# Performance work log

Measured on AMD Instinct MI355X. Metric: run time of the kernel, lower is better.

The kernel has to match this reference:

```python
import jax, jax.numpy as jnp
import numpy as np


def _hippo_dplr(n):
    # HiPPO-LegS -> NPLR -> DPLR (diagonal plus low rank) init, as in S4
    pr = np.sqrt(1.0 + 2.0 * np.arange(n))
    A = -(np.tril(pr[:, None] * pr[None, :]) - np.diag(np.arange(n)))
    p = np.sqrt(np.arange(n) + 0.5)
    b = np.sqrt(2.0 * np.arange(n) + 1.0)
    S = A + p[:, None] * p[None, :]
    lam_re = np.full(n, np.mean(np.diagonal(S)))
    lam_im, V = np.linalg.eigh(S * -1j)  # S*-1j is Hermitian
    p_c = V.conj().T @ p.astype(np.complex128)
    b_c = V.conj().T @ b.astype(np.complex128)
    return lam_re, lam_im, p_c, b_c


def setup_inputs():
    B, L, H, N = 4, 1024, 512, 64
    key = jax.random.key(0)
    kx, kc, ks, k1, k2 = jax.random.split(key, 5)
    lam_re, lam_im, p_c, b_c = _hippo_dplr(N)
    c = jax.random.normal(kc, (N, 2)) * (0.5 ** 0.5)
    f32 = lambda a: jnp.asarray(a, dtype=jnp.float32)
    return {
        'x': jax.random.normal(kx, (B, L, H), dtype=jnp.float32),
        'norm_weight': jnp.ones((H,), jnp.float32),
        'norm_bias': jnp.zeros((H,), jnp.float32),
        'lambda_re': f32(lam_re), 'lambda_im': f32(lam_im),
        'p_re': f32(p_c.real), 'p_im': f32(p_c.imag),
        'b_re': f32(b_c.real), 'b_im': f32(b_c.imag),
        'c_re': c[:, 0].astype(jnp.float32), 'c_im': c[:, 1].astype(jnp.float32),
        'd': jnp.ones((), jnp.float32),
        'log_step': jax.random.uniform(ks, (), jnp.float32, float(np.log(0.001)), float(np.log(0.1))),
        'out_w': (jax.random.normal(k1, (H, H), jnp.float32) / np.sqrt(H)).astype(jnp.float32),
        'out_b': jnp.zeros((H,), jnp.float32),
        'out2_w': (jax.random.normal(k2, (H, H), jnp.float32) / np.sqrt(H)).astype(jnp.float32),
        'out2_b': jnp.zeros((H,), jnp.float32),
    }


def reference(x, norm_weight, norm_bias, lambda_re, lambda_im, p_re, p_im,
              b_re, b_im, c_re, c_im, d, log_step, out_w, out_b, out2_w, out2_b):
    Bsz, L, H = x.shape
    skip = x
    # LayerNorm over channel dim (eps=1e-5, eqx default)
    mu = jnp.mean(x, -1, keepdims=True)
    var = jnp.mean((x - mu) ** 2, -1, keepdims=True)
    xn = (x - mu) / jnp.sqrt(var + 1e-5) * norm_weight + norm_bias
    # --- S4 DPLR bilinear discretization ---
    lam = (lambda_re + 1j * lambda_im).astype(jnp.complex64)
    p = (p_re + 1j * p_im).astype(jnp.complex64)
    b = (b_re + 1j * b_im).astype(jnp.complex64)
    c = (c_re + 1j * c_im).astype(jnp.complex64)
    step = jnp.exp(log_step).astype(jnp.complex64)
    N = lam.shape[0]
    I = jnp.eye(N, dtype=jnp.complex64)
    A = jnp.diag(lam) - p[:, None] * p[None, :].conj()
    A0 = (2.0 / step) * I + A
    Dinv = jnp.diag(1.0 / ((2.0 / step) - lam))
    qcD = p.conj()[None, :] @ Dinv           # [1,N]
    Dp = Dinv @ p[:, None]                   # [N,1]
    A1 = Dinv - (Dp @ qcD) / (1.0 + (qcD @ p[:, None]))  # Woodbury
    Ab = A1 @ A0                             # [N,N] discrete state matrix
    Bb = 2.0 * (A1 @ b[:, None])[:, 0]       # [N]
    # --- sequential state-space scan over time, vectorized over (B,H) lanes ---
    u = xn.astype(jnp.complex64)             # [B,L,H]

    def step_fn(state, u_t):                 # state: [B,H,N], u_t: [B,H]
        new = jnp.einsum('nm,bhm->bhn', Ab, state) + u_t[..., None] * Bb
        return new, jnp.einsum('n,bhn->bh', c, new).real

    init = jnp.zeros((Bsz, H, N), jnp.complex64)
    _, ys = jax.lax.scan(step_fn, init, jnp.moveaxis(u, 1, 0))  # ys: [L,B,H]
    y = jnp.moveaxis(ys, 0, 1) + d * xn      # feedthrough term
    # --- GELU + GLU-style gated output projection, residual ---
    y = jax.nn.gelu(y)
    gate = jax.nn.sigmoid(y @ out2_w.T + out2_b)
    return skip + (y @ out_w.T + out_b) * gate
```

## Files before the change

kernel.cpp:

```cpp
#include <hip/hip_runtime.h>
#include <hip/hip_bf16.h>
#include <math.h>

#define HDIM 512
#define LSEQ 1024
#define BSZ  4

typedef __attribute__((ext_vector_type(8))) short short8;
typedef __attribute__((ext_vector_type(4))) float floatx4;

__device__ __forceinline__ float2 cmul(float2 a, float2 b) {
  float2 r;
  r.x = a.x * b.x - a.y * b.y;
  r.y = a.x * b.y + a.y * b.x;
  return r;
}
__device__ __forceinline__ float2 cadd(float2 a, float2 b) {
  float2 r; r.x = a.x + b.x; r.y = a.y + b.y; return r;
}
__device__ __forceinline__ float2 cfma(float2 a, float2 b, float2 c) {
  c.x += a.x * b.x - a.y * b.y;
  c.y += a.x * b.y + a.y * b.x;
  return c;
}
__device__ __forceinline__ ushort f2bf(float f) {
  __hip_bfloat16 h = __float2bfloat16(f);
  return *(ushort*)&h;
}

__global__ __launch_bounds__(256) void ln_kernel(const float* __restrict__ x,
    const float* __restrict__ w, const float* __restrict__ b, float* __restrict__ xn) {
  int row = blockIdx.x * 4 + (threadIdx.x >> 6);
  int lane = threadIdx.x & 63;
  const float* xr = x + (size_t)row * HDIM;
  float4 v0 = ((const float4*)xr)[lane];
  float4 v1 = ((const float4*)xr)[lane + 64];
  float s  = v0.x + v0.y + v0.z + v0.w + v1.x + v1.y + v1.z + v1.w;
  float ss = v0.x*v0.x + v0.y*v0.y + v0.z*v0.z + v0.w*v0.w
           + v1.x*v1.x + v1.y*v1.y + v1.z*v1.z + v1.w*v1.w;
  #pragma unroll
  for (int m = 1; m < 64; m <<= 1) { s += __shfl_xor(s, m); ss += __shfl_xor(ss, m); }
  float mu   = s * (1.0f / HDIM);
  float var  = ss * (1.0f / HDIM) - mu * mu;
  float rstd = rsqrtf(var + 1e-5f);
  float4 w0 = ((const float4*)w)[lane];
  float4 w1 = ((const float4*)w)[lane + 64];
  float4 b0 = ((const float4*)b)[lane];
  float4 b1 = ((const float4*)b)[lane + 64];
  float4 o0, o1;
  o0.x = (v0.x - mu) * rstd * w0.x + b0.x;
  o0.y = (v0.y - mu) * rstd * w0.y + b0.y;
  o0.z = (v0.z - mu) * rstd * w0.z + b0.z;
  o0.w = (v0.w - mu) * rstd * w0.w + b0.w;
  o1.x = (v1.x - mu) * rstd * w1.x + b1.x;
  o1.y = (v1.y - mu) * rstd * w1.y + b1.y;
  o1.z = (v1.z - mu) * rstd * w1.z + b1.z;
  o1.w = (v1.w - mu) * rstd * w1.w + b1.w;
  float* xo = xn + (size_t)row * HDIM;
  ((float4*)xo)[lane] = o0;
  ((float4*)xo)[lane + 64] = o1;
}

__global__ __launch_bounds__(512) void kgen_kernel(
    const float* __restrict__ lre, const float* __restrict__ lim,
    const float* __restrict__ pre, const float* __restrict__ pim,
    const float* __restrict__ bre, const float* __restrict__ bim,
    const float* __restrict__ cre, const float* __restrict__ cim,
    const float* __restrict__ logstep, float* __restrict__ Kout) {
  __shared__ float2 Ldab[64], Lu[64], Lr[64], LBb[64];
  __shared__ float2 P[8][64];
  __shared__ float2 M32[4096];
  __shared__ float2 Rv[2048];
  __shared__ float2 Wv[2048];
  int tid = threadIdx.x;
  int j = tid & 63;
  int p = tid >> 6;

  if (tid < 64) {
    int n = tid;
    float step = expf(logstep[0]);
    float g = 2.0f / step;
    float lr = lre[n], li = lim[n];
    float pr = pre[n], pi = pim[n];
    float br = bre[n], bi = bim[n];
    float den  = (g - lr) * (g - lr) + li * li;
    float dinr = (g - lr) / den, dini = li / den;
    float dabr = (g + lr) * dinr - li * dini;
    float dabi = (g + lr) * dini + li * dinr;
    float ur = dinr * pr - dini * pi;
    float ui = dinr * pi + dini * pr;
    float qr = pr * dinr + pi * dini;
    float qi = pr * dini - pi * dinr;
    float pm2 = pr * pr + pi * pi;
    float betr = pm2 * dinr, beti = pm2 * dini;
    float gar = qr * br - qi * bi;
    float gai = qr * bi + qi * br;
    #pragma unroll
    for (int m = 1; m < 64; m <<= 1) {
      betr += __shfl_xor(betr, m); beti += __shfl_xor(beti, m);
      gar  += __shfl_xor(gar, m);  gai  += __shfl_xor(gai, m);
    }
    float obr = 1.0f + betr, obi = beti;
    float ob2 = obr * obr + obi * obi;
    float kr = -2.0f * g * obr / ob2;
    float ki =  2.0f * g * obi / ob2;
    float rr = kr * qr - ki * qi;
    float ri = kr * qi + ki * qr;
    float tgr = (gar * obr + gai * obi) / ob2;
    float tgi = (gai * obr - gar * obi) / ob2;
    float dbr = dinr * br - dini * bi;
    float dbi = dinr * bi + dini * br;
    float Bbr = 2.0f * (dbr - (ur * tgr - ui * tgi));
    float Bbi = 2.0f * (dbi - (ur * tgi + ui * tgr));
    float2 t;
    t.x = dabr; t.y = dabi; Ldab[n] = t;
    t.x = ur;   t.y = ui;   Lu[n]   = t;
    t.x = rr;   t.y = ri;   Lr[n]   = t;
    t.x = Bbr;  t.y = Bbi;  LBb[n]  = t;
  }
  __syncthreads();

  float2 dab[8], u[8], rn[8], cv[8];
  #pragma unroll
  for (int ii = 0; ii < 8; ii++) {
    int n = p * 8 + ii;
    dab[ii] = Ldab[n]; u[ii] = Lu[n]; rn[ii] = Lr[n];
  }
  float2 rj = Lr[j];
  #pragma unroll
  for (int ii = 0; ii < 8; ii++) {
    int n = p * 8 + ii;
    cv[ii] = cmul(u[ii], rj);
    if (n == j) cv[ii] = cadd(cv[ii], dab[ii]);
  }
  for (int s = 0; s < 31; s++) {
    float2 part; part.x = 0.f; part.y = 0.f;
    #pragma unroll
    for (int ii = 0; ii < 8; ii++) part = cfma(rn[ii], cv[ii], part);
    P[p][j] = part;
    __syncthreads();
    float2 d; d.x = 0.f; d.y = 0.f;
    #pragma unroll
    for (int q = 0; q < 8; q++) d = cadd(d, P[q][j]);
    __syncthreads();
    #pragma unroll
    for (int ii = 0; ii < 8; ii++) {
      float2 nc = cmul(dab[ii], cv[ii]);
      nc = cfma(u[ii], d, nc);
      cv[ii] = nc;
    }
  }
  #pragma unroll
  for (int ii = 0; ii < 8; ii++) M32[(p * 8 + ii) * 64 + j] = cv[ii];
  if (tid < 64) { float2 cc; cc.x = cre[tid]; cc.y = cim[tid]; Rv[tid] = cc; }
  __syncthreads();

  float2 Mreg[8];
  #pragma unroll
  for (int ii = 0; ii < 8; ii++) Mreg[ii] = M32[(p * 8 + ii) * 64 + j];
  for (int a = 1; a < 32; a++) {
    float2 part; part.x = 0.f; part.y = 0.f;
    #pragma unroll
    for (int ii = 0; ii < 8; ii++) {
      float2 Rk = Rv[(a - 1) * 64 + p * 8 + ii];
      part = cfma(Rk, Mreg[ii], part);
    }
    P[p][j] = part;
    __syncthreads();
    if (p == 0) {
      float2 d; d.x = 0.f; d.y = 0.f;
      #pragma unroll
      for (int q = 0; q < 8; q++) d = cadd(d, P[q][j]);
      Rv[a * 64 + j] = d;
    }
    __syncthreads();
  }

  if (tid < 64) {
    int n = tid;
    float2 dab0 = Ldab[n], u0 = Lu[n], r0 = Lr[n];
    float2 w = LBb[n];
    Wv[n * 32 + 0] = w;
    for (int b = 1; b < 32; b++) {
      float dr = r0.x * w.x - r0.y * w.y;
      float di = r0.x * w.y + r0.y * w.x;
      #pragma unroll
      for (int m = 1; m < 64; m <<= 1) { dr += __shfl_xor(dr, m); di += __shfl_xor(di, m); }
      float2 nw;
      nw.x = dab0.x * w.x - dab0.y * w.y + u0.x * dr - u0.y * di;
      nw.y = dab0.x * w.y + dab0.y * w.x + u0.x * di + u0.y * dr;
      w = nw;
      Wv[n * 32 + b] = w;
    }
  }
  __syncthreads();

  #pragma unroll
  for (int q = 0; q < 2; q++) {
    int midx = q * 512 + tid;
    int a = midx >> 5, b = midx & 31;
    float acc = 0.f;
    for (int n = 0; n < 64; n++) {
      float2 R = Rv[a * 64 + n];
      float2 W = Wv[n * 32 + b];
      acc += R.x * W.x - R.y * W.y;
    }
    Kout[midx] = acc;
  }
}

__global__ __launch_bounds__(256) void prep_kernel(
    const float* __restrict__ xn, const float* __restrict__ K,
    const float* __restrict__ w1, const float* __restrict__ w2,
    ushort* __restrict__ Uhi, ushort* __restrict__ Ulo,
    ushort* __restrict__ Thi, ushort* __restrict__ Tlo,
    ushort* __restrict__ Wst) {
  __shared__ float tile[64][65];
  int blk = blockIdx.x;
  int tid = threadIdx.x;
  if (blk < 512) {
    int ht = blk & 7, lt = (blk >> 3) & 15, b = blk >> 7;
    #pragma unroll
    for (int q = 0; q < 16; q++) {
      int idx = q * 256 + tid;
      int r = idx >> 6, c = idx & 63;
      tile[r][c] = xn[((size_t)(b * LSEQ + lt * 64 + r)) * HDIM + ht * 64 + c];
    }
    __syncthreads();
    #pragma unroll
    for (int q = 0; q < 16; q++) {
      int idx = q * 256 + tid;
      int r = idx >> 6, c = idx & 63;
      float v = tile[c][r];
      ushort h = f2bf(v);
      float rem = v - __bfloat162float(*(__hip_bfloat16*)&h);
      ushort l = f2bf(rem);
      size_t off = ((size_t)(b * HDIM + ht * 64 + r)) * LSEQ + lt * 64 + c;
      Uhi[off] = h;
      Ulo[off] = l;
    }
  } else if (blk < 768) {
    int e0 = ((blk - 512) * 256 + tid) * 8;
    int n = e0 >> 9, k0 = e0 & 511;
    const float* Wr = (n < 512) ? (w1 + (size_t)n * 512 + k0)
                                : (w2 + (size_t)(n - 512) * 512 + k0);
    ushort tmp[8];
    #pragma unroll
    for (int t = 0; t < 8; t++) tmp[t] = f2bf(Wr[t]);
    *(short8*)&Wst[e0] = *(short8*)tmp;
  } else {
    int r = blk - 768;
    int t = r * 2 + (tid >> 7);
    int tau0 = (tid & 127) * 8;
    ushort hi[8], lo[8];
    #pragma unroll
    for (int q = 0; q < 8; q++) {
      int tau = tau0 + q;
      float v = (tau <= t) ? K[t - tau] : 0.f;
      hi[q] = f2bf(v);
      float rem = v - __bfloat162float(*(__hip_bfloat16*)&hi[q]);
      lo[q] = f2bf(rem);
    }
    *(short8*)&Thi[(size_t)t * 1024 + tau0] = *(short8*)hi;
    *(short8*)&Tlo[(size_t)t * 1024 + tau0] = *(short8*)lo;
  }
}

__global__ __launch_bounds__(256) void conv_gemm_kernel(
    const ushort* __restrict__ Thi, const ushort* __restrict__ Tlo,
    const ushort* __restrict__ Uhi, const ushort* __restrict__ Ulo,
    const float* __restrict__ xn, const float* __restrict__ dptr,
    __hip_bfloat16* __restrict__ A) {
  __shared__ ushort sTh[64 * 40];
  __shared__ ushort sTl[64 * 40];
  __shared__ ushort sUh[64 * 40];
  __shared__ ushort sUl[64 * 40];
  int tid = threadIdx.x;
  int lane = tid & 63;
  int wv = tid >> 6;
  int wm = wv >> 1, wn = wv & 1;
  int by = blockIdx.y;
  int bm = (by < 8) ? by : 23 - by;
  int bn = blockIdx.x;
  floatx4 acc[2][2] = {};
  int srow = tid >> 2;
  int scol = (tid & 3) * 8;
  int fr = lane & 15, fq = (lane >> 4) * 8;
  size_t Toff = (size_t)(bm * 64 + srow) * 1024 + scol;
  size_t Uoff = (size_t)(bn * 64 + srow) * 1024 + scol;
  int KT = 2 * (bm + 1);
  for (int kt = 0; kt < KT; kt++) {
    int k0 = kt * 32;
    *(uint4*)&sTh[srow * 40 + scol] = *(const uint4*)&Thi[Toff + k0];
    *(uint4*)&sTl[srow * 40 + scol] = *(const uint4*)&Tlo[Toff + k0];
    *(uint4*)&sUh[srow * 40 + scol] = *(const uint4*)&Uhi[Uoff + k0];
    *(uint4*)&sUl[srow * 40 + scol] = *(const uint4*)&Ulo[Uoff + k0];
    __syncthreads();
    short8 ah[2], al[2], bh[2], bl[2];
    #pragma unroll
    for (int i = 0; i < 2; i++) {
      ah[i] = *(const short8*)&sTh[(wm * 32 + i * 16 + fr) * 40 + fq];
      al[i] = *(const short8*)&sTl[(wm * 32 + i * 16 + fr) * 40 + fq];
      bh[i] = *(const short8*)&sUh[(wn * 32 + i * 16 + fr) * 40 + fq];
      bl[i] = *(const short8*)&sUl[(wn * 32 + i * 16 + fr) * 40 + fq];
    }
    #pragma unroll
    for (int i = 0; i < 2; i++)
      #pragma unroll
      for (int j = 0; j < 2; j++) {
        acc[i][j] = __builtin_amdgcn_mfma_f32_16x16x32_bf16(ah[i], bh[j], acc[i][j], 0, 0, 0);
        acc[i][j] = __builtin_amdgcn_mfma_f32_16x16x32_bf16(al[i], bh[j], acc[i][j], 0, 0, 0);
        acc[i][j] = __builtin_amdgcn_mfma_f32_16x16x32_bf16(ah[i], bl[j], acc[i][j], 0, 0, 0);
      }
    __syncthreads();
  }
  float d = dptr[0];
  int row0 = bm * 64 + wm * 32;
  int col0 = bn * 64 + wn * 32;
  int fc = lane & 15, frq = (lane >> 4) * 4;
  #pragma unroll
  for (int i = 0; i < 2; i++)
    #pragma unroll
    for (int j = 0; j < 2; j++)
      #pragma unroll
      for (int r = 0; r < 4; r++) {
        int t = row0 + i * 16 + frq + r;
        int c = col0 + j * 16 + fc;
        int b = c >> 9, h = c & 511;
        size_t off = (size_t)(b * LSEQ + t) * HDIM + h;
        float y = acc[i][j][r] + d * xn[off];
        float tnh = tanhf(0.7978845608028654f * (y + 0.044715f * y * y * y));
        A[off] = __float2bfloat16(0.5f * y * (1.0f + tnh));
      }
}

__global__ __launch_bounds__(256) void proj_kernel(
    const __hip_bfloat16* __restrict__ Abuf, const ushort* __restrict__ Wst,
    const float* __restrict__ x, const float* __restrict__ ob,
    const float* __restrict__ o2b, float* __restrict__ out) {
  __shared__ ushort sA[64 * 40];
  __shared__ ushort sW1[64 * 40];
  __shared__ ushort sW2[64 * 40];
  int tid = threadIdx.x;
  int lane = tid & 63;
  int wv = tid >> 6;
  int wm = wv >> 1, wn = wv & 1;
  int bm = blockIdx.y, bn = blockIdx.x;
  int srow = tid >> 2;
  int scol = (tid & 3) * 8;
  int fr = lane & 15, fq = (lane >> 4) * 8;
  floatx4 acc1[2][2] = {}, acc2[2][2] = {};
  const ushort* Ab = (const ushort*)Abuf;
  size_t Aoff  = (size_t)(bm * 64 + srow) * 512 + scol;
  size_t W1off = (size_t)(bn * 64 + srow) * 512 + scol;
  size_t W2off = W1off + (size_t)512 * 512;
  for (int kt = 0; kt < 16; kt++) {
    int k0 = kt * 32;
    *(uint4*)&sA[srow * 40 + scol]  = *(const uint4*)&Ab[Aoff + k0];
    *(uint4*)&sW1[srow * 40 + scol] = *(const uint4*)&Wst[W1off + k0];
    *(uint4*)&sW2[srow * 40 + scol] = *(const uint4*)&Wst[W2off + k0];
    __syncthreads();
    short8 af[2], b1[2], b2[2];
    #pragma unroll
    for (int i = 0; i < 2; i++) {
      af[i] = *(const short8*)&sA[(wm * 32 + i * 16 + fr) * 40 + fq];
      b1[i] = *(const short8*)&sW1[(wn * 32 + i * 16 + fr) * 40 + fq];
      b2[i] = *(const short8*)&sW2[(wn * 32 + i * 16 + fr) * 40 + fq];
    }
    #pragma unroll
    for (int i = 0; i < 2; i++)
      #pragma unroll
      for (int j = 0; j < 2; j++) {
        acc1[i][j] = __builtin_amdgcn_mfma_f32_16x16x32_bf16(af[i], b1[j], acc1[i][j], 0, 0, 0);
        acc2[i][j] = __builtin_amdgcn_mfma_f32_16x16x32_bf16(af[i], b2[j], acc2[i][j], 0, 0, 0);
      }
    __syncthreads();
  }
  int row0 = bm * 64 + wm * 32;
  int col0 = bn * 64 + wn * 32;
  int fc = lane & 15, frq = (lane >> 4) * 4;
  #pragma unroll
  for (int i = 0; i < 2; i++)
    #pragma unroll
    for (int j = 0; j < 2; j++)
      #pragma unroll
      for (int r = 0; r < 4; r++) {
        int row = row0 + i * 16 + frq + r;
        int col = col0 + j * 16 + fc;
        float c1 = acc1[i][j][r] + ob[col];
        float c2 = acc2[i][j][r] + o2b[col];
        float gate = 1.0f / (1.0f + expf(-c2));
        size_t off = (size_t)row * HDIM + col;
        out[off] = x[off] + c1 * gate;
      }
}

extern "C" void kernel_launch(void* const* d_in, const int* in_sizes, int n_in,
                              void* d_out, int out_size, void* d_ws, size_t ws_size,
                              hipStream_t stream) {
  const float* x   = (const float*)d_in[0];
  const float* nw  = (const float*)d_in[1];
  const float* nb  = (const float*)d_in[2];
  const float* lre = (const float*)d_in[3];
  const float* lim = (const float*)d_in[4];
  const float* pre = (const float*)d_in[5];
  const float* pim = (const float*)d_in[6];
  const float* bre = (const float*)d_in[7];
  const float* bim = (const float*)d_in[8];
  const float* cre = (const float*)d_in[9];
  const float* cim = (const float*)d_in[10];
  const float* dsc = (const float*)d_in[11];
  const float* lst = (const float*)d_in[12];
  const float* w1  = (const float*)d_in[13];
  const float* ob  = (const float*)d_in[14];
  const float* w2  = (const float*)d_in[15];
  const float* o2b = (const float*)d_in[16];

  char* ws = (char*)d_ws;
  float* xn    = (float*)(ws);
  ushort* Uhi  = (ushort*)(ws + (size_t)(8  << 20));
  ushort* Ulo  = (ushort*)(ws + (size_t)(12 << 20));
  ushort* Thi  = (ushort*)(ws + (size_t)(16 << 20));
  ushort* Tlo  = (ushort*)(ws + (size_t)(18 << 20));
  ushort* Wst  = (ushort*)(ws + (size_t)(20 << 20));
  __hip_bfloat16* Abuf = (__hip_bfloat16*)(ws + (size_t)(21 << 20));
  float* Kbuf  = (float*)(ws + (size_t)(25 << 20));
  float* out   = (float*)d_out;

  ln_kernel<<<dim3(1024), dim3(256), 0, stream>>>(x, nw, nb, xn);
  kgen_kernel<<<dim3(1), dim3(512), 0, stream>>>(lre, lim, pre, pim, bre, bim,
                                                 cre, cim, lst, Kbuf);
  prep_kernel<<<dim3(1280), dim3(256), 0, stream>>>(xn, Kbuf, w1, w2,
                                                    Uhi, Ulo, Thi, Tlo, Wst);
  conv_gemm_kernel<<<dim3(32, 16), dim3(256), 0, stream>>>(Thi, Tlo, Uhi, Ulo,
                                                           xn, dsc, Abuf);
  proj_kernel<<<dim3(8, 64), dim3(256), 0, stream>>>(Abuf, Wst, x, ob, o2b, out);
}
```

Measured before the change: 183.6 us.

## Fuse layernorm and kernel generation into one launch with shuffle reductions

Merges the layernorm kernel and the single-block SSM kernel-generation kernel into one launch: block 0 computes the convolution kernel while the remaining blocks run layernorm, nine rows per block. Inside kernel generation, the matrix-power and projection reductions now use 8-lane shuffles instead of shared-memory partials with two barriers per step, and the W-vector recurrence runs on a ninth wave concurrently with the matrix power. The aim is to remove one launch and to overlap the serial single-block work with the bandwidth-bound layernorm. The cost is an irregular 576-thread block shape that may limit occupancy for the layernorm blocks.

```diff
diff --git a/kernel.cpp b/kernel.cpp
--- a/kernel.cpp
+++ b/kernel.cpp
@@ -28,53 +28,53 @@
   return *(ushort*)&h;
 }
 
-__global__ __launch_bounds__(256) void ln_kernel(const float* __restrict__ x,
-    const float* __restrict__ w, const float* __restrict__ b, float* __restrict__ xn) {
-  int row = blockIdx.x * 4 + (threadIdx.x >> 6);
-  int lane = threadIdx.x & 63;
-  const float* xr = x + (size_t)row * HDIM;
-  float4 v0 = ((const float4*)xr)[lane];
-  float4 v1 = ((const float4*)xr)[lane + 64];
-  float s  = v0.x + v0.y + v0.z + v0.w + v1.x + v1.y + v1.z + v1.w;
-  float ss = v0.x*v0.x + v0.y*v0.y + v0.z*v0.z + v0.w*v0.w
-           + v1.x*v1.x + v1.y*v1.y + v1.z*v1.z + v1.w*v1.w;
-  #pragma unroll
-  for (int m = 1; m < 64; m <<= 1) { s += __shfl_xor(s, m); ss += __shfl_xor(ss, m); }
-  float mu   = s * (1.0f / HDIM);
-  float var  = ss * (1.0f / HDIM) - mu * mu;
-  float rstd = rsqrtf(var + 1e-5f);
-  float4 w0 = ((const float4*)w)[lane];
-  float4 w1 = ((const float4*)w)[lane + 64];
-  float4 b0 = ((const float4*)b)[lane];
-  float4 b1 = ((const float4*)b)[lane + 64];
-  float4 o0, o1;
-  o0.x = (v0.x - mu) * rstd * w0.x + b0.x;
-  o0.y = (v0.y - mu) * rstd * w0.y + b0.y;
-  o0.z = (v0.z - mu) * rstd * w0.z + b0.z;
-  o0.w = (v0.w - mu) * rstd * w0.w + b0.w;
-  o1.x = (v1.x - mu) * rstd * w1.x + b1.x;
-  o1.y = (v1.y - mu) * rstd * w1.y + b1.y;
-  o1.z = (v1.z - mu) * rstd * w1.z + b1.z;
-  o1.w = (v1.w - mu) * rstd * w1.w + b1.w;
-  float* xo = xn + (size_t)row * HDIM;
-  ((float4*)xo)[lane] = o0;
-  ((float4*)xo)[lane + 64] = o1;
-}
-
-__global__ __launch_bounds__(512) void kgen_kernel(
+__global__ __launch_bounds__(576) void stage1_kernel(
+    const float* __restrict__ x, const float* __restrict__ nw,
+    const float* __restrict__ nb, float* __restrict__ xn,
     const float* __restrict__ lre, const float* __restrict__ lim,
     const float* __restrict__ pre, const float* __restrict__ pim,
     const float* __restrict__ bre, const float* __restrict__ bim,
     const float* __restrict__ cre, const float* __restrict__ cim,
     const float* __restrict__ logstep, float* __restrict__ Kout) {
   __shared__ float2 Ldab[64], Lu[64], Lr[64], LBb[64];
-  __shared__ float2 P[8][64];
-  __shared__ float2 M32[4096];
   __shared__ float2 Rv[2048];
   __shared__ float2 Wv[2048];
   int tid = threadIdx.x;
-  int j = tid & 63;
-  int p = tid >> 6;
+  int wv = tid >> 6;
+  int lane = tid & 63;
+
+  if (blockIdx.x != 0) {
+    int row = (blockIdx.x - 1) * 9 + wv;
+    if (row >= BSZ * LSEQ) return;
+    const float* xr = x + (size_t)row * HDIM;
+    float4 v0 = ((const float4*)xr)[lane];
+    float4 v1 = ((const float4*)xr)[lane + 64];
+    float s  = v0.x + v0.y + v0.z + v0.w + v1.x + v1.y + v1.z + v1.w;
+    float ss = v0.x*v0.x + v0.y*v0.y + v0.z*v0.z + v0.w*v0.w
+             + v1.x*v1.x + v1.y*v1.y + v1.z*v1.z + v1.w*v1.w;
+    #pragma unroll
+    for (int m = 1; m < 64; m <<= 1) { s += __shfl_xor(s, m); ss += __shfl_xor(ss, m); }
+    float mu   = s * (1.0f / HDIM);
+    float var  = ss * (1.0f / HDIM) - mu * mu;
+    float rstd = rsqrtf(var + 1e-5f);
+    float4 w0 = ((const float4*)nw)[lane];
+    float4 w1 = ((const float4*)nw)[lane + 64];
+    float4 b0 = ((const float4*)nb)[lane];
+    float4 b1 = ((const float4*)nb)[lane + 64];
+    float4 o0, o1;
+    o0.x = (v0.x - mu) * rstd * w0.x + b0.x;
+    o0.y = (v0.y - mu) * rstd * w0.y + b0.y;
+    o0.z = (v0.z - mu) * rstd * w0.z + b0.z;
+    o0.w = (v0.w - mu) * rstd * w0.w + b0.w;
+    o1.x = (v1.x - mu) * rstd * w1.x + b1.x;
+    o1.y = (v1.y - mu) * rstd * w1.y + b1.y;
+    o1.z = (v1.z - mu) * rstd * w1.z + b1.z;
+    o1.w = (v1.w - mu) * rstd * w1.w + b1.w;
+    float* xo = xn + (size_t)row * HDIM;
+    ((float4*)xo)[lane] = o0;
+    ((float4*)xo)[lane + 64] = o1;
+    return;
+  }
 
   if (tid < 64) {
     int n = tid;
@@ -118,86 +118,80 @@
     t.x = rr;   t.y = ri;   Lr[n]   = t;
     t.x = Bbr;  t.y = Bbi;  LBb[n]  = t;
   }
+  if (wv == 8) { float2 cc; cc.x = cre[lane]; cc.y = cim[lane]; Rv[lane] = cc; }
   __syncthreads();
 
-  float2 dab[8], u[8], rn[8], cv[8];
-  #pragma unroll
-  for (int ii = 0; ii < 8; ii++) {
-    int n = p * 8 + ii;
-    dab[ii] = Ldab[n]; u[ii] = Lu[n]; rn[ii] = Lr[n];
-  }
-  float2 rj = Lr[j];
-  #pragma unroll
-  for (int ii = 0; ii < 8; ii++) {
-    int n = p * 8 + ii;
-    cv[ii] = cmul(u[ii], rj);
-    if (n == j) cv[ii] = cadd(cv[ii], dab[ii]);
-  }
-  for (int s = 0; s < 31; s++) {
-    float2 part; part.x = 0.f; part.y = 0.f;
-    #pragma unroll
-    for (int ii = 0; ii < 8; ii++) part = cfma(rn[ii], cv[ii], part);
-    P[p][j] = part;
-    __syncthreads();
-    float2 d; d.x = 0.f; d.y = 0.f;
-    #pragma unroll
-    for (int q = 0; q < 8; q++) d = cadd(d, P[q][j]);
-    __syncthreads();
+  int g8 = lane >> 3;
+  int q8 = lane & 7;
+  int jm = wv * 8 + g8;
+  float2 cv[8];
+
+  if (wv < 8) {
+    float2 dab[8], u[8], rn[8];
     #pragma unroll
     for (int ii = 0; ii < 8; ii++) {
-      float2 nc = cmul(dab[ii], cv[ii]);
-      nc = cfma(u[ii], d, nc);
-      cv[ii] = nc;
-    }
-  }
-  #pragma unroll
-  for (int ii = 0; ii < 8; ii++) M32[(p * 8 + ii) * 64 + j] = cv[ii];
-  if (tid < 64) { float2 cc; cc.x = cre[tid]; cc.y = cim[tid]; Rv[tid] = cc; }
-  __syncthreads();
-
-  float2 Mreg[8];
-  #pragma unroll
-  for (int ii = 0; ii < 8; ii++) Mreg[ii] = M32[(p * 8 + ii) * 64 + j];
-  for (int a = 1; a < 32; a++) {
-    float2 part; part.x = 0.f; part.y = 0.f;
+      int n = q8 * 8 + ii;
+      dab[ii] = Ldab[n]; u[ii] = Lu[n]; rn[ii] = Lr[n];
+    }
+    float2 rj = Lr[jm];
     #pragma unroll
     for (int ii = 0; ii < 8; ii++) {
-      float2 Rk = Rv[(a - 1) * 64 + p * 8 + ii];
-      part = cfma(Rk, Mreg[ii], part);
-    }
-    P[p][j] = part;
-    __syncthreads();
-    if (p == 0) {
-      float2 d; d.x = 0.f; d.y = 0.f;
-      #pragma unroll
-      for (int q = 0; q < 8; q++) d = cadd(d, P[q][j]);
-      Rv[a * 64 + j] = d;
-    }
-    __syncthreads();
-  }
-
-  if (tid < 64) {
-    int n = tid;
-    float2 dab0 = Ldab[n], u0 = Lu[n], r0 = Lr[n];
-    float2 w = LBb[n];
-    Wv[n * 32 + 0] = w;
+      int n = q8 * 8 + ii;
+      cv[ii] = cmul(u[ii], rj);
+      if (n == jm) cv[ii] = cadd(cv[ii], dab[ii]);
+    }
+    for (int s = 0; s < 31; s++) {
+      float2 part; part.x = 0.f; part.y = 0.f;
+      #pragma unroll
+      for (int ii = 0; ii < 8; ii++) part = cfma(rn[ii], cv[ii], part);
+      #pragma unroll
+      for (int m = 1; m < 8; m <<= 1) {
+        part.x += __shfl_xor(part.x, m);
+        part.y += __shfl_xor(part.y, m);
+      }
+      #pragma unroll
+      for (int ii = 0; ii < 8; ii++) {
+        float2 nc = cmul(dab[ii], cv[ii]);
+        cv[ii] = cfma(u[ii], part, nc);
+      }
+    }
+  } else {
+    float2 dab0 = Ldab[lane], u0 = Lu[lane], r0 = Lr[lane];
+    float2 w = LBb[lane];
+    Wv[lane * 32 + 0] = w;
     for (int b = 1; b < 32; b++) {
       float dr = r0.x * w.x - r0.y * w.y;
       float di = r0.x * w.y + r0.y * w.x;
       #pragma unroll
       for (int m = 1; m < 64; m <<= 1) { dr += __shfl_xor(dr, m); di += __shfl_xor(di, m); }
-      float2 nw;
-      nw.x = dab0.x * w.x - dab0.y * w.y + u0.x * dr - u0.y * di;
-      nw.y = dab0.x * w.y + dab0.y * w.x + u0.x * di + u0.y * dr;
-      w = nw;
-      Wv[n * 32 + b] = w;
+      float2 nw2;
+      nw2.x = dab0.x * w.x - dab0.y * w.y + u0.x * dr - u0.y * di;
+      nw2.y = dab0.x * w.y + dab0.y * w.x + u0.x * di + u0.y * dr;
+      w = nw2;
+      Wv[lane * 32 + b] = w;
     }
   }
   __syncthreads();
 
-  #pragma unroll
-  for (int q = 0; q < 2; q++) {
-    int midx = q * 512 + tid;
+  for (int a = 1; a < 32; a++) {
+    if (wv < 8) {
+      float2 part; part.x = 0.f; part.y = 0.f;
+      #pragma unroll
+      for (int ii = 0; ii < 8; ii++) {
+        float2 Rk = Rv[(a - 1) * 64 + q8 * 8 + ii];
+        part = cfma(Rk, cv[ii], part);
+      }
+      #pragma unroll
+      for (int m = 1; m < 8; m <<= 1) {
+        part.x += __shfl_xor(part.x, m);
+        part.y += __shfl_xor(part.y, m);
+      }
+      if (q8 == 0) Rv[a * 64 + jm] = part;
+    }
+    __syncthreads();
+  }
+
+  for (int midx = tid; midx < 1024; midx += 576) {
     int a = midx >> 5, b = midx & 31;
     float acc = 0.f;
     for (int n = 0; n < 64; n++) {
@@ -427,9 +421,9 @@
   float* Kbuf  = (float*)(ws + (size_t)(25 << 20));
   float* out   = (float*)d_out;
 
-  ln_kernel<<<dim3(1024), dim3(256), 0, stream>>>(x, nw, nb, xn);
-  kgen_kernel<<<dim3(1), dim3(512), 0, stream>>>(lre, lim, pre, pim, bre, bim,
-                                                 cre, cim, lst, Kbuf);
+  stage1_kernel<<<dim3(457), dim3(576), 0, stream>>>(x, nw, nb, xn,
+                                                     lre, lim, pre, pim, bre, bim,
+                                                     cre, cim, lst, Kbuf);
   prep_kernel<<<dim3(1280), dim3(256), 0, stream>>>(xn, Kbuf, w1, w2,
                                                     Uhi, Ulo, Thi, Tlo, Wst);
   conv_gemm_kernel<<<dim3(32, 16), dim3(256), 0, stream>>>(Thi, Tlo, Uhi, Ulo,
```

Result: faster. 172.1 us (-6.2%).
